# Kernel tuning notes

Measured on AMD Instinct MI355X. Metric: run time of the kernel, lower is better.

The kernel has to match this reference:

```python
import jax, jax.numpy as jnp
import numpy as np

B, T, D, R = 16, 4096, 512, 256

# Buffers (match torch: linspace(0,T-1,R).long() truncates toward zero)
_LANDMARKS = np.linspace(0.0, T - 1, R).astype(np.int64)
_POS = np.arange(T)[:, None]                                   # [T,1]
_MASK = (_LANDMARKS[None, :] < _POS)                           # [T,R] bool: landmark j < position i
_TDIST = np.clip((_POS.astype(np.float32) - _LANDMARKS[None, :].astype(np.float32)) / T, 0.0, None).astype(np.float32)  # [T,R]


def setup_inputs() -> dict:
    key = jax.random.key(0)
    k1, k2, k3 = jax.random.split(key, 3)
    return {
        "z": jax.random.normal(k1, (B, T, D), dtype=jnp.float32),
        "gegenbauer_weights": jax.random.normal(k2, (3,), dtype=jnp.float32),
        "temporal_alpha": jax.random.normal(k3, (1,), dtype=jnp.float32),
    }


def reference(z, gegenbauer_weights, temporal_alpha):
    dtype = z.dtype
    mask = jnp.asarray(_MASK)                       # [T,R]
    tdist = jnp.asarray(_TDIST, dtype=dtype)        # [T,R]
    lm = jnp.asarray(_LANDMARKS)                    # [R]

    # F.normalize(z, dim=-1) with eps=1e-12
    norm = jnp.linalg.norm(z, axis=-1, keepdims=True)
    Q = z / jnp.maximum(norm, 1e-12)                # [B,T,D]
    K = Q[:, lm, :]                                 # [B,R,D]
    C = jnp.einsum('btd,brd->btr', Q, K)            # [B,T,R] cosine similarity

    # Gegenbauer mixture
    alpha = jax.nn.softmax(gegenbauer_weights)
    C2 = C * C
    P1 = (1.0 + C) * 0.5
    P2 = (3.0 * C2 - 1.0) * 0.5
    P3 = (5.0 * C2 * C - 3.0 * C) * 0.5
    Phi = alpha[0] * P1 + alpha[1] * P2 + alpha[2] * P3

    # Causal mask
    Phi = Phi * mask.astype(dtype)[None, :, :]

    # Temporal decay
    a_td = jax.nn.softplus(temporal_alpha[0])
    Phi = Phi * jnp.exp(-a_td * tdist)[None, :, :]

    # Row-sum normalization
    row_sum = jnp.maximum(Phi.sum(axis=-1, keepdims=True), 1e-6)
    Phi = Phi / row_sum

    # Append constant-ones feature -> [B,T,R+1]
    ones = jnp.ones((Phi.shape[0], Phi.shape[1], 1), dtype=dtype)
    return jnp.concatenate([Phi, ones], axis=-1)
```

## Files before the change

kernel.cpp:

```cpp
#include <hip/hip_runtime.h>
#include <hip/hip_bf16.h>
#include <math.h>

#define B_DIM 16
#define T_DIM 4096
#define D_DIM 512
#define R_DIM 256

#define TM 128
#define BK 32
#define LDP 40
#define NKCH (D_DIM/BK)

typedef __bf16 bf16x8 __attribute__((ext_vector_type(8)));
typedef float floatx4 __attribute__((ext_vector_type(4)));

__device__ __forceinline__ int landmark_of(int r) {
    if (r >= 255) return 4095;
    const double step = 4095.0 / 255.0;
    return (int)((double)r * step);
}

__device__ __forceinline__ void split_bf16(float x, __bf16& h, __bf16& l) {
    h = (__bf16)x;
    l = (__bf16)(x - (float)h);
}

__global__ void nystrom_prep_kernel(const float* __restrict__ z,
                                    __bf16* __restrict__ Khi, __bf16* __restrict__ Klo) {
    int blk = blockIdx.x;
    int b = blk >> 8;
    int r = blk & 255;
    int lane = threadIdx.x;
    int lm = landmark_of(r);
    const float* src = z + ((size_t)b * T_DIM + lm) * D_DIM + lane * 8;
    float4 v0 = ((const float4*)src)[0];
    float4 v1 = ((const float4*)src)[1];
    float ss = v0.x*v0.x + v0.y*v0.y + v0.z*v0.z + v0.w*v0.w
             + v1.x*v1.x + v1.y*v1.y + v1.z*v1.z + v1.w*v1.w;
    #pragma unroll
    for (int off = 1; off < 64; off <<= 1) ss += __shfl_xor(ss, off, 64);
    float inv = 1.0f / fmaxf(sqrtf(ss), 1e-12f);
    float q[8] = {v0.x*inv, v0.y*inv, v0.z*inv, v0.w*inv,
                  v1.x*inv, v1.y*inv, v1.z*inv, v1.w*inv};
    bf16x8 oh, ol;
    #pragma unroll
    for (int j = 0; j < 8; j++) { __bf16 h, l; split_bf16(q[j], h, l); oh[j] = h; ol[j] = l; }
    size_t dst = (((size_t)b * NKCH + (lane >> 2)) * R_DIM + r) * BK + (size_t)(lane & 3) * 8;
    *(bf16x8*)(Khi + dst) = oh;
    *(bf16x8*)(Klo + dst) = ol;
}

__global__ __launch_bounds__(256, 2)
void nystrom_main_kernel(const float* __restrict__ z,
                         const __bf16* __restrict__ Khi, const __bf16* __restrict__ Klo,
                         const float* __restrict__ gw, const float* __restrict__ ta,
                         float* __restrict__ out) {
    __shared__ __attribute__((aligned(16))) char smem[61440];
    __shared__ int   lmtab[R_DIM];
    __shared__ float elmtab[R_DIM];

    __bf16* Ash = (__bf16*)(smem);
    __bf16* Asl = (__bf16*)(smem + 10240);
    __bf16* Bsh = (__bf16*)(smem + 20480);
    __bf16* Bsl = (__bf16*)(smem + 40960);
    float* red    = (float*)(smem);
    float* rnormp = (float*)(smem + 1024);
    float* rinvp  = (float*)(smem + 1536);
    float* rspart = (float*)(smem + 2048);

    const int tid  = threadIdx.x;
    const int b    = blockIdx.y;
    const int t0   = blockIdx.x * TM;
    const int lane = tid & 63;
    const int wv   = tid >> 6;
    const int quad = lane >> 4;
    const int ln   = lane & 15;

    float g0 = gw[0], g1 = gw[1], g2 = gw[2];
    float gm = fmaxf(g0, fmaxf(g1, g2));
    float e0 = expf(g0 - gm), e1 = expf(g1 - gm), e2 = expf(g2 - gm);
    float esum = e0 + e1 + e2;
    float al0 = e0 / esum, al1 = e1 / esum, al2 = e2 / esum;
    float ax = ta[0];
    float a_td = (ax > 20.f) ? ax : log1pf(expf(ax));

    {
        int lm = landmark_of(tid);
        lmtab[tid] = lm;
        elmtab[tid] = expf(a_td * (float)lm * (1.0f / 4096.0f));
    }

    const int srowA = tid >> 1;
    const int scolA = (tid & 1) * 16;
    const float* zrow = z + ((size_t)b * T_DIM + (t0 + srowA)) * D_DIM + scolA;
    const size_t bbase = (size_t)b * NKCH * R_DIM * BK;

    floatx4 acc[8][4];
    #pragma unroll
    for (int i = 0; i < 8; i++)
        #pragma unroll
        for (int j = 0; j < 4; j++) acc[i][j] = (floatx4){0.f, 0.f, 0.f, 0.f};
    float ssq = 0.0f;

    float4 a0, a1, a2, a3;
    uint4 h0, h1, h2, h3, l0, l1, l2, l3;
    {
        const float4* ap = (const float4*)(zrow);
        a0 = ap[0]; a1 = ap[1]; a2 = ap[2]; a3 = ap[3];
        const uint4* ph = (const uint4*)(Khi + bbase + (size_t)tid * BK);
        const uint4* pl = (const uint4*)(Klo + bbase + (size_t)tid * BK);
        h0 = ph[0]; h1 = ph[1]; h2 = ph[2]; h3 = ph[3];
        l0 = pl[0]; l1 = pl[1]; l2 = pl[2]; l3 = pl[3];
    }

    #pragma unroll 1
    for (int kt = 0; kt < D_DIM; kt += BK) {
        float av[16] = {a0.x,a0.y,a0.z,a0.w, a1.x,a1.y,a1.z,a1.w,
                        a2.x,a2.y,a2.z,a2.w, a3.x,a3.y,a3.z,a3.w};
        #pragma unroll
        for (int j = 0; j < 16; j++) ssq += av[j] * av[j];
        bf16x8 ph0, pl0, ph1, pl1;
        #pragma unroll
        for (int j = 0; j < 8; j++) { __bf16 h, l; split_bf16(av[j],   h, l); ph0[j]=h; pl0[j]=l; }
        #pragma unroll
        for (int j = 0; j < 8; j++) { __bf16 h, l; split_bf16(av[8+j], h, l); ph1[j]=h; pl1[j]=l; }
        *(bf16x8*)&Ash[srowA * LDP + scolA]     = ph0;
        *(bf16x8*)&Ash[srowA * LDP + scolA + 8] = ph1;
        *(bf16x8*)&Asl[srowA * LDP + scolA]     = pl0;
        *(bf16x8*)&Asl[srowA * LDP + scolA + 8] = pl1;
        {
            uint4* dh = (uint4*)((char*)Bsh + tid * (LDP * 2));
            uint4* dl = (uint4*)((char*)Bsl + tid * (LDP * 2));
            dh[0] = h0; dh[1] = h1; dh[2] = h2; dh[3] = h3;
            dl[0] = l0; dl[1] = l1; dl[2] = l2; dl[3] = l3;
        }
        __syncthreads();
        if (kt + BK < D_DIM) {
            const float4* ap = (const float4*)(zrow + kt + BK);
            a0 = ap[0]; a1 = ap[1]; a2 = ap[2]; a3 = ap[3];
            size_t coff = bbase + (size_t)((kt >> 5) + 1) * R_DIM * BK + (size_t)tid * BK;
            const uint4* ph = (const uint4*)(Khi + coff);
            const uint4* pl = (const uint4*)(Klo + coff);
            h0 = ph[0]; h1 = ph[1]; h2 = ph[2]; h3 = ph[3];
            l0 = pl[0]; l1 = pl[1]; l2 = pl[2]; l3 = pl[3];
        }
        {
            const int koff = quad * 8;
            bf16x8 bfh[4], bfl[4];
            #pragma unroll
            for (int ni = 0; ni < 4; ni++) {
                int rrow = wv * 64 + ni * 16 + ln;
                bfh[ni] = *(const bf16x8*)&Bsh[rrow * LDP + koff];
                bfl[ni] = *(const bf16x8*)&Bsl[rrow * LDP + koff];
            }
            #pragma unroll
            for (int mi = 0; mi < 8; mi++) {
                bf16x8 afh = *(const bf16x8*)&Ash[(mi * 16 + ln) * LDP + koff];
                bf16x8 afl = *(const bf16x8*)&Asl[(mi * 16 + ln) * LDP + koff];
                #pragma unroll
                for (int ni = 0; ni < 4; ni++) {
                    acc[mi][ni] = __builtin_amdgcn_mfma_f32_16x16x32_bf16(
                        afh, bfh[ni], acc[mi][ni], 0, 0, 0);
                    acc[mi][ni] = __builtin_amdgcn_mfma_f32_16x16x32_bf16(
                        afh, bfl[ni], acc[mi][ni], 0, 0, 0);
                    acc[mi][ni] = __builtin_amdgcn_mfma_f32_16x16x32_bf16(
                        afl, bfh[ni], acc[mi][ni], 0, 0, 0);
                }
            }
        }
        __syncthreads();
    }

    red[tid] = ssq;
    __syncthreads();
    if (tid < TM) {
        float s = red[tid * 2] + red[tid * 2 + 1];
        rnormp[tid] = 1.0f / fmaxf(sqrtf(s), 1e-12f);
    }
    __syncthreads();

    int   lm_r[4];
    float elm_r[4];
    #pragma unroll
    for (int ni = 0; ni < 4; ni++) {
        int r = wv * 64 + ni * 16 + ln;
        lm_r[ni]  = lmtab[r];
        elm_r[ni] = elmtab[r];
    }

    #pragma unroll
    for (int mi = 0; mi < 8; mi++) {
        #pragma unroll
        for (int reg = 0; reg < 4; reg++) {
            int row = mi * 16 + quad * 4 + reg;
            int t = t0 + row;
            float rn = rnormp[row];
            float e_t = expf(-a_td * (float)t * (1.0f / 4096.0f));
            float s = 0.f;
            #pragma unroll
            for (int ni = 0; ni < 4; ni++) {
                float phi = 0.f;
                if (lm_r[ni] < t) {
                    float c  = acc[mi][ni][reg] * rn;
                    float c2 = c * c;
                    float P1 = 0.5f * (1.f + c);
                    float P2 = 0.5f * (3.f * c2 - 1.f);
                    float P3 = 0.5f * (5.f * c2 * c - 3.f * c);
                    float p  = al0 * P1 + al1 * P2 + al2 * P3;
                    phi = p * e_t * elm_r[ni];
                }
                acc[mi][ni][reg] = phi;
                s += phi;
            }
            #pragma unroll
            for (int off = 1; off < 16; off <<= 1) s += __shfl_xor(s, off, 64);
            if (ln == 0) rspart[wv * TM + row] = s;
        }
    }
    __syncthreads();
    if (tid < TM) {
        float rs = rspart[0 * TM + tid] + rspart[1 * TM + tid]
                 + rspart[2 * TM + tid] + rspart[3 * TM + tid];
        rinvp[tid] = 1.0f / fmaxf(rs, 1e-6f);
    }
    __syncthreads();

    float* ob = out + ((size_t)b * T_DIM + t0) * 257;
    #pragma unroll
    for (int mi = 0; mi < 8; mi++) {
        #pragma unroll
        for (int reg = 0; reg < 4; reg++) {
            int row = mi * 16 + quad * 4 + reg;
            float inv = rinvp[row];
            #pragma unroll
            for (int ni = 0; ni < 4; ni++) {
                int r = wv * 64 + ni * 16 + ln;
                ob[(size_t)row * 257 + r] = acc[mi][ni][reg] * inv;
            }
        }
    }
    if (tid < TM) ob[(size_t)tid * 257 + 256] = 1.0f;
}

extern "C" void kernel_launch(void* const* d_in, const int* in_sizes, int n_in,
                              void* d_out, int out_size, void* d_ws, size_t ws_size,
                              hipStream_t stream) {
    const float* z  = (const float*)d_in[0];
    const float* gw = (const float*)d_in[1];
    const float* ta = (const float*)d_in[2];
    float* out = (float*)d_out;
    __bf16* Khi = (__bf16*)d_ws;
    __bf16* Klo = (__bf16*)((char*)d_ws + (size_t)B_DIM * R_DIM * D_DIM * 2);

    nystrom_prep_kernel<<<dim3(B_DIM * R_DIM), 64, 0, stream>>>(z, Khi, Klo);
    nystrom_main_kernel<<<dim3(T_DIM / TM, B_DIM), 256, 0, stream>>>(z, Khi, Klo, gw, ta, out);
}
```

Baseline: 252.1 us.

## Load landmark fragments directly from global in MFMA layout, double K-step per stage

The prep kernel now writes the normalized landmark hi/lo bf16 splits in a fragment-major layout, so each wave lane can load its B-operand fragments straight from global memory (L2-resident) without staging them through shared memory. This removes the B shared-memory stores and reads and shrinks LDS use. The K tile is doubled to 64, which halves the number of barriers per block. The cost is global loads issued inside the MFMA loop with no prefetch, plus more registers for the larger A staging.

```diff
diff --git a/kernel.cpp b/kernel.cpp
--- a/kernel.cpp
+++ b/kernel.cpp
@@ -8,9 +8,9 @@
 #define R_DIM 256
 
 #define TM 128
-#define BK 32
-#define LDP 40
-#define NKCH (D_DIM/BK)
+#define BK 64
+#define LDP 72
+#define NKS (D_DIM/32)
 
 typedef __bf16 bf16x8 __attribute__((ext_vector_type(8)));
 typedef float floatx4 __attribute__((ext_vector_type(4)));
@@ -46,7 +46,8 @@
     bf16x8 oh, ol;
     #pragma unroll
     for (int j = 0; j < 8; j++) { __bf16 h, l; split_bf16(q[j], h, l); oh[j] = h; ol[j] = l; }
-    size_t dst = (((size_t)b * NKCH + (lane >> 2)) * R_DIM + r) * BK + (size_t)(lane & 3) * 8;
+    size_t dst = ((((size_t)b * NKS + (lane >> 2)) * 16 + (r >> 4)) * 64
+                  + (size_t)(lane & 3) * 16 + (r & 15)) * 8;
     *(bf16x8*)(Khi + dst) = oh;
     *(bf16x8*)(Klo + dst) = ol;
 }
@@ -56,14 +57,12 @@
                          const __bf16* __restrict__ Khi, const __bf16* __restrict__ Klo,
                          const float* __restrict__ gw, const float* __restrict__ ta,
                          float* __restrict__ out) {
-    __shared__ __attribute__((aligned(16))) char smem[61440];
+    __shared__ __attribute__((aligned(16))) char smem[36864];
     __shared__ int   lmtab[R_DIM];
     __shared__ float elmtab[R_DIM];
 
     __bf16* Ash = (__bf16*)(smem);
-    __bf16* Asl = (__bf16*)(smem + 10240);
-    __bf16* Bsh = (__bf16*)(smem + 20480);
-    __bf16* Bsl = (__bf16*)(smem + 40960);
+    __bf16* Asl = (__bf16*)(smem + 18432);
     float* red    = (float*)(smem);
     float* rnormp = (float*)(smem + 1024);
     float* rinvp  = (float*)(smem + 1536);
@@ -92,9 +91,13 @@
     }
 
     const int srowA = tid >> 1;
-    const int scolA = (tid & 1) * 16;
+    const int scolA = (tid & 1) * 32;
     const float* zrow = z + ((size_t)b * T_DIM + (t0 + srowA)) * D_DIM + scolA;
-    const size_t bbase = (size_t)b * NKCH * R_DIM * BK;
+
+    const size_t kfoff = (size_t)b * (NKS * 16 * 64 * 8)
+                       + (size_t)wv * 2048 + (size_t)lane * 8;
+    const __bf16* khb = Khi + kfoff;
+    const __bf16* klb = Klo + kfoff;
 
     floatx4 acc[8][4];
     #pragma unroll
@@ -103,57 +106,51 @@
         for (int j = 0; j < 4; j++) acc[i][j] = (floatx4){0.f, 0.f, 0.f, 0.f};
     float ssq = 0.0f;
 
-    float4 a0, a1, a2, a3;
-    uint4 h0, h1, h2, h3, l0, l1, l2, l3;
+    float4 a0, a1, a2, a3, a4, a5, a6, a7;
     {
         const float4* ap = (const float4*)(zrow);
         a0 = ap[0]; a1 = ap[1]; a2 = ap[2]; a3 = ap[3];
-        const uint4* ph = (const uint4*)(Khi + bbase + (size_t)tid * BK);
-        const uint4* pl = (const uint4*)(Klo + bbase + (size_t)tid * BK);
-        h0 = ph[0]; h1 = ph[1]; h2 = ph[2]; h3 = ph[3];
-        l0 = pl[0]; l1 = pl[1]; l2 = pl[2]; l3 = pl[3];
+        a4 = ap[4]; a5 = ap[5]; a6 = ap[6]; a7 = ap[7];
     }
 
     #pragma unroll 1
     for (int kt = 0; kt < D_DIM; kt += BK) {
-        float av[16] = {a0.x,a0.y,a0.z,a0.w, a1.x,a1.y,a1.z,a1.w,
-                        a2.x,a2.y,a2.z,a2.w, a3.x,a3.y,a3.z,a3.w};
-        #pragma unroll
-        for (int j = 0; j < 16; j++) ssq += av[j] * av[j];
-        bf16x8 ph0, pl0, ph1, pl1;
-        #pragma unroll
-        for (int j = 0; j < 8; j++) { __bf16 h, l; split_bf16(av[j],   h, l); ph0[j]=h; pl0[j]=l; }
-        #pragma unroll
-        for (int j = 0; j < 8; j++) { __bf16 h, l; split_bf16(av[8+j], h, l); ph1[j]=h; pl1[j]=l; }
-        *(bf16x8*)&Ash[srowA * LDP + scolA]     = ph0;
-        *(bf16x8*)&Ash[srowA * LDP + scolA + 8] = ph1;
-        *(bf16x8*)&Asl[srowA * LDP + scolA]     = pl0;
-        *(bf16x8*)&Asl[srowA * LDP + scolA + 8] = pl1;
-        {
-            uint4* dh = (uint4*)((char*)Bsh + tid * (LDP * 2));
-            uint4* dl = (uint4*)((char*)Bsl + tid * (LDP * 2));
-            dh[0] = h0; dh[1] = h1; dh[2] = h2; dh[3] = h3;
-            dl[0] = l0; dl[1] = l1; dl[2] = l2; dl[3] = l3;
+        float av[32] = {a0.x,a0.y,a0.z,a0.w, a1.x,a1.y,a1.z,a1.w,
+                        a2.x,a2.y,a2.z,a2.w, a3.x,a3.y,a3.z,a3.w,
+                        a4.x,a4.y,a4.z,a4.w, a5.x,a5.y,a5.z,a5.w,
+                        a6.x,a6.y,a6.z,a6.w, a7.x,a7.y,a7.z,a7.w};
+        #pragma unroll
+        for (int j = 0; j < 32; j++) ssq += av[j] * av[j];
+        #pragma unroll
+        for (int g = 0; g < 4; g++) {
+            bf16x8 ph, pl;
+            #pragma unroll
+            for (int j = 0; j < 8; j++) {
+                __bf16 h, l; split_bf16(av[g*8+j], h, l); ph[j] = h; pl[j] = l;
+            }
+            *(bf16x8*)&Ash[srowA * LDP + scolA + g*8] = ph;
+            *(bf16x8*)&Asl[srowA * LDP + scolA + g*8] = pl;
         }
         __syncthreads();
+
         if (kt + BK < D_DIM) {
             const float4* ap = (const float4*)(zrow + kt + BK);
             a0 = ap[0]; a1 = ap[1]; a2 = ap[2]; a3 = ap[3];
-            size_t coff = bbase + (size_t)((kt >> 5) + 1) * R_DIM * BK + (size_t)tid * BK;
-            const uint4* ph = (const uint4*)(Khi + coff);
-            const uint4* pl = (const uint4*)(Klo + coff);
-            h0 = ph[0]; h1 = ph[1]; h2 = ph[2]; h3 = ph[3];
-            l0 = pl[0]; l1 = pl[1]; l2 = pl[2]; l3 = pl[3];
-        }
-        {
-            const int koff = quad * 8;
-            bf16x8 bfh[4], bfl[4];
+            a4 = ap[4]; a5 = ap[5]; a6 = ap[6]; a7 = ap[7];
+        }
+
+        const int ksb = kt >> 5;
+        #pragma unroll
+        for (int s = 0; s < 2; s++) {
+            const __bf16* khp = khb + (size_t)(ksb + s) * 8192;
+            const __bf16* klp = klb + (size_t)(ksb + s) * 8192;
+            bf16x8 bh[4], bl[4];
             #pragma unroll
             for (int ni = 0; ni < 4; ni++) {
-                int rrow = wv * 64 + ni * 16 + ln;
-                bfh[ni] = *(const bf16x8*)&Bsh[rrow * LDP + koff];
-                bfl[ni] = *(const bf16x8*)&Bsl[rrow * LDP + koff];
-            }
+                bh[ni] = *(const bf16x8*)(khp + ni * 512);
+                bl[ni] = *(const bf16x8*)(klp + ni * 512);
+            }
+            const int koff = s * 32 + quad * 8;
             #pragma unroll
             for (int mi = 0; mi < 8; mi++) {
                 bf16x8 afh = *(const bf16x8*)&Ash[(mi * 16 + ln) * LDP + koff];
@@ -161,11 +158,11 @@
                 #pragma unroll
                 for (int ni = 0; ni < 4; ni++) {
                     acc[mi][ni] = __builtin_amdgcn_mfma_f32_16x16x32_bf16(
-                        afh, bfh[ni], acc[mi][ni], 0, 0, 0);
+                        afh, bh[ni], acc[mi][ni], 0, 0, 0);
                     acc[mi][ni] = __builtin_amdgcn_mfma_f32_16x16x32_bf16(
-                        afh, bfl[ni], acc[mi][ni], 0, 0, 0);
+                        afh, bl[ni], acc[mi][ni], 0, 0, 0);
                     acc[mi][ni] = __builtin_amdgcn_mfma_f32_16x16x32_bf16(
-                        afl, bfh[ni], acc[mi][ni], 0, 0, 0);
+                        afl, bh[ni], acc[mi][ni], 0, 0, 0);
                 }
             }
         }
```

After: 270.1 us. +7.1%, slower.
